# Optimization experiments

Hardware: AMD Instinct MI355X
Metric: run time of the kernel (lower is better)

The kernel has to match this reference:

```python
import jax, jax.numpy as jnp
import numpy as np

D = 768
B = 32
N = 768


def setup_inputs() -> dict:
    key = jax.random.key(0)
    k1, k2, k3, k4 = jax.random.split(key, 4)
    stdv = 1.0 / np.sqrt(D)
    X = jax.random.normal(k1, (B, N, D), dtype=jnp.float32)
    adj = jax.random.uniform(k2, (B, N, N), dtype=jnp.float32)
    W_l = jax.random.uniform(k3, (D, D), dtype=jnp.float32, minval=-stdv, maxval=stdv)
    W_l1 = jax.random.uniform(k4, (D, D), dtype=jnp.float32, minval=-stdv, maxval=stdv)
    return {"X": X, "adj": adj, "W_l": W_l, "W_l1": W_l1}


def _row_normalize(adj):
    # rowsum^-1 with inf -> 0 (rows summing to zero stay zero)
    rowsum = adj.sum(axis=-1, keepdims=True)  # [B, N, 1]
    r_inv = jnp.where(rowsum == 0, 0.0, 1.0 / rowsum)
    return adj * r_inv


def reference(X, adj, W_l, W_l1):
    # X: [B, N, D], adj: [B, N, N]
    adj_n = _row_normalize(adj)
    e1 = jnp.einsum('bnd,de->bne', X, W_l1)        # message transform
    e11 = jnp.einsum('bnm,bmd->bnd', adj_n, e1)    # aggregate
    X1 = jnp.einsum('bnd,de->bne', X, W_l)         # self transform
    h = X1 + e11
    return jax.nn.leaky_relu(h, negative_slope=0.01)
```

## Files before the change

kernel.cpp:

```cpp
#include <hip/hip_runtime.h>
#include <hip/hip_bf16.h>
#include <cstdint>
#include <cstddef>

#define BN_ROWS 24576
#define DD 768
#define BE (768*768)
#define BM 192
#define BN_T 192
#define BK 32
#define ABUF 12288
#define BUFSZ 24576

typedef __attribute__((ext_vector_type(8))) short bf16x8;
typedef __attribute__((ext_vector_type(4))) float f32x4;
typedef __attribute__((ext_vector_type(8))) unsigned short u16x8;

static __device__ __forceinline__ unsigned short f2bf(float f) {
  unsigned int u = __builtin_bit_cast(unsigned int, f);
  unsigned int lsb = (u >> 16) & 1u;
  u += 0x7fffu + lsb;
  return (unsigned short)(u >> 16);
}



#define PREP_CX 4096
#define PREP_WT 144
#define PREP_FL 288
#define PREP_AN 6144

__global__ __launch_bounds__(256) void prep(const float* __restrict__ X,
                                            const float* __restrict__ adj,
                                            const float* __restrict__ Wl,
                                            const float* __restrict__ Wl1,
                                            unsigned short* __restrict__ Xb,
                                            unsigned short* __restrict__ adjnb,
                                            unsigned short* __restrict__ WlT,
                                            unsigned short* __restrict__ Wl1T) {
  __shared__ float tile[64][65];
  const int bid = blockIdx.x;

  if (bid < PREP_CX) {
    const int n4 = (BN_ROWS * DD) / 4;
    for (int i = bid * 256 + threadIdx.x; i < n4; i += PREP_CX * 256) {
      float4 v = reinterpret_cast<const float4*>(X)[i];
      ushort4 o;
      o.x = f2bf(v.x); o.y = f2bf(v.y); o.z = f2bf(v.z); o.w = f2bf(v.w);
      reinterpret_cast<ushort4*>(Xb)[i] = o;
    }
  } else if (bid < PREP_CX + PREP_WT) {
    const int tb = bid - PREP_CX;
    const int tr = tb / 12, tc = tb % 12;
    const int c = threadIdx.x & 63, r0 = threadIdx.x >> 6;
    #pragma unroll
    for (int i = 0; i < 16; ++i) {
      int r = r0 + i * 4;
      tile[r][c] = Wl1[(size_t)(tr * 64 + r) * DD + tc * 64 + c];
    }
    __syncthreads();
    #pragma unroll
    for (int i = 0; i < 16; ++i) {
      int r2 = r0 + i * 4;
      Wl1T[(size_t)(tc * 64 + r2) * DD + tr * 64 + c] = f2bf(tile[c][r2]);
    }
  } else if (bid < PREP_CX + PREP_WT + PREP_FL) {
    const int b2 = bid - (PREP_CX + PREP_WT);
    const int wg = b2 * 4 + (threadIdx.x >> 6);
    const int lane = threadIdx.x & 63;
    const int d0 = (wg % 96) * 8;
    const int e = (wg / 96) * 64 + lane;
    u16x8 o;
    #pragma unroll
    for (int j = 0; j < 8; ++j)
      o[j] = f2bf(Wl[(size_t)(d0 + j) * DD + e]);
    const int base = ((e >> 4) * 24 + (d0 >> 5)) * 512
                   + ((e & 15) + (((d0 >> 3) & 3) << 4)) * 8;
    *reinterpret_cast<u16x8*>(WlT + base) = o;
  } else {
    const int rb = bid - (PREP_CX + PREP_WT + PREP_FL);
    const int wid = threadIdx.x >> 6, lane = threadIdx.x & 63;
    const int row = rb * 4 + wid;
    const float4* a = reinterpret_cast<const float4*>(adj + (size_t)row * DD);
    float4 v[3];
    float s = 0.f;
    #pragma unroll
    for (int i = 0; i < 3; ++i) {
      v[i] = a[i * 64 + lane];
      s += (v[i].x + v[i].y) + (v[i].z + v[i].w);
    }
    #pragma unroll
    for (int off = 32; off; off >>= 1) s += __shfl_down(s, off);
    s = __shfl(s, 0);
    float rinv = (s == 0.f) ? 0.f : 1.f / s;
    ushort4* o = reinterpret_cast<ushort4*>(adjnb + (size_t)row * DD);
    #pragma unroll
    for (int i = 0; i < 3; ++i) {
      ushort4 u;
      u.x = f2bf(v[i].x * rinv); u.y = f2bf(v[i].y * rinv);
      u.z = f2bf(v[i].z * rinv); u.w = f2bf(v[i].w * rinv);
      o[i * 64 + lane] = u;
    }
  }
}

__global__ __launch_bounds__(256, 2) void gemm_e1(
    const unsigned short* __restrict__ Xb,
    const unsigned short* __restrict__ W1T,
    unsigned short* __restrict__ e1T)
{
  __shared__ char smem[2 * BUFSZ];
  constexpr int NT = 24;
  const int tid = threadIdx.x, lane = tid & 63;
  const int wid = tid >> 6;
  const int wr = wid >> 1, wc = wid & 1;

  const int logical = (blockIdx.x & 7) * 64 + (blockIdx.x >> 3);
  const int mt = logical >> 2, nt = logical & 3;
  const int b = mt >> 2;
  const unsigned short* Ab0 = Xb + (size_t)mt * BM * DD;
  const unsigned short* Bb0 = W1T + (size_t)nt * BN_T * DD;

  const int r_in = lane >> 2;
  const int s_in = lane & 3;

  auto stage = [&](int s) {
    const int buf = (s & 1) * BUFSZ;
    #pragma unroll
    for (int i = 0; i < 6; ++i) {
      int chunk = wid * 6 + i;
      bool isA = chunk < 12;
      int c = isA ? chunk : chunk - 12;
      int row = c * 16 + r_in;
      int slot = s_in ^ ((row >> 1) & 3);
      const unsigned short* src = (isA ? Ab0 : Bb0) + (size_t)row * DD + s * BK + slot * 8;
      __builtin_amdgcn_global_load_lds(
          (const __attribute__((address_space(1))) void*)src,
          (__attribute__((address_space(3))) void*)(smem + buf + (isA ? 0 : ABUF) + c * 1024),
          16, 0, 0);
    }
  };

  const int ks = lane >> 4;
  auto frag = [&](int off, int row) -> bf16x8 {
    int slot = ks ^ ((row >> 1) & 3);
    return *reinterpret_cast<const bf16x8*>(smem + off + row * 64 + slot * 16);
  };

  f32x4 acc[6][6] = {};
  const int arow = wr * 96 + (lane & 15);
  const int brow = wc * 96 + (lane & 15);

  stage(0);
  for (int t = 0; t < NT; ++t) {
    asm volatile("s_waitcnt vmcnt(0)" ::: "memory");
    __builtin_amdgcn_s_barrier();
    if (t + 1 < NT) stage(t + 1);
    const int bufA = (t & 1) * BUFSZ;
    const int bufB = bufA + ABUF;
    bf16x8 a[6], bg[6];
    #pragma unroll
    for (int i = 0; i < 6; ++i) a[i] = frag(bufA, arow + i * 16);
    #pragma unroll
    for (int i = 0; i < 6; ++i) bg[i] = frag(bufB, brow + i * 16);
    __builtin_amdgcn_s_setprio(1);
    #pragma unroll
    for (int ni = 0; ni < 6; ++ni)
      #pragma unroll
      for (int mi = 0; mi < 6; ++mi)
        acc[mi][ni] = __builtin_amdgcn_mfma_f32_16x16x32_bf16(a[mi], bg[ni], acc[mi][ni], 0, 0, 0);
    __builtin_amdgcn_s_setprio(0);
  }

  unsigned short* ob = e1T + (size_t)b * BE;
  const int m0 = (mt & 3) * BM + wr * 96 + (lane >> 4) * 4;
  const int l15 = lane & 15;
  #pragma unroll
  for (int mi = 0; mi < 6; ++mi)
    #pragma unroll
    for (int ni = 0; ni < 6; ++ni) {
      int m = m0 + mi * 16;
      int cb = nt * 12 + wc * 6 + ni;
      int fa = (cb * 24 + (m >> 5)) * 512
             + (l15 + (((m >> 3) & 3) << 4)) * 8 + (m & 7);
      f32x4 v = acc[mi][ni];
      ushort4 o;
      o.x = f2bf(v[0]); o.y = f2bf(v[1]); o.z = f2bf(v[2]); o.w = f2bf(v[3]);
      *reinterpret_cast<ushort4*>(ob + fa) = o;
    }
}

__global__ __launch_bounds__(256, 2) void gemm_bg(
    const unsigned short* __restrict__ adjnb,
    const unsigned short* __restrict__ e1T,
    const unsigned short* __restrict__ Xb,
    const unsigned short* __restrict__ WlT,
    float* __restrict__ out)
{
  __shared__ char smem[24576];
  constexpr int NT = 48;
  const int tid = threadIdx.x, lane = tid & 63;
  const int wid = tid >> 6;
  const int wr = wid >> 1, wc = wid & 1;

  const int logical = (blockIdx.x & 7) * 64 + (blockIdx.x >> 3);
  const int b = logical >> 4;
  const int r = logical & 15;
  const int mt = r >> 2, nt = r & 3;
  const size_t bo = (size_t)b * BE;
  const unsigned short* A0 = adjnb + bo + (size_t)mt * BM * DD;
  const unsigned short* A1 = Xb + bo + (size_t)mt * BM * DD;
  const unsigned short* B0 = e1T + bo;
  const unsigned short* B1 = WlT;

  const int r_in = lane >> 2;
  const int s_in = lane & 3;
  const int colblk0 = nt * 12 + wc * 6;

  auto stage = [&](int s) {
    int sc = s < NT ? s : 0;
    const unsigned short* base = (sc >= 24) ? A1 : A0;
    int kk = (sc >= 24) ? sc - 24 : sc;
    const int buf = (s & 1) * 12288;
    #pragma unroll
    for (int i = 0; i < 3; ++i) {
      int chunk = wid * 3 + i;
      int row = chunk * 16 + r_in;
      int slot = s_in ^ ((row >> 1) & 3);
      const unsigned short* src = base + (size_t)row * DD + kk * BK + slot * 8;
      __builtin_amdgcn_global_load_lds(
          (const __attribute__((address_space(1))) void*)src,
          (__attribute__((address_space(3))) void*)(smem + buf + chunk * 1024),
          16, 0, 0);
    }
  };

  auto loadB = [&](int s, bf16x8* dst) {
    int sc = s < NT ? s : 0;
    const unsigned short* base = (sc >= 24) ? B1 : B0;
    int kk = (sc >= 24) ? sc - 24 : sc;
    #pragma unroll
    for (int ni = 0; ni < 6; ++ni)
      dst[ni] = *reinterpret_cast<const bf16x8*>(
          base + ((colblk0 + ni) * 24 + kk) * 512 + lane * 8);
  };

  const int ks = lane >> 4;
  auto rdA = [&](int off, int row) -> bf16x8 {
    int slot = ks ^ ((row >> 1) & 3);
    return *reinterpret_cast<const bf16x8*>(smem + off + row * 64 + slot * 16);
  };

  f32x4 acc[6][6] = {};
  const int arow = wr * 96 + (lane & 15);
  bf16x8 bA[6], bB[6];

  auto body = [&](int bufo, bf16x8* bfr) {
    #pragma unroll
    for (int mh = 0; mh < 2; ++mh) {
      bf16x8 a[3];
      #pragma unroll
      for (int i = 0; i < 3; ++i) a[i] = rdA(bufo, arow + mh * 48 + i * 16);
      __builtin_amdgcn_s_setprio(1);
      #pragma unroll
      for (int mi = 0; mi < 3; ++mi)
        #pragma unroll
        for (int ni = 0; ni < 6; ++ni)
          acc[mh * 3 + mi][ni] = __builtin_amdgcn_mfma_f32_16x16x32_bf16(
              a[mi], bfr[ni], acc[mh * 3 + mi][ni], 0, 0, 0);
      __builtin_amdgcn_s_setprio(0);
    }
  };

  stage(0); loadB(0, bA);
  for (int t = 0; t < NT; t += 2) {
    asm volatile("s_waitcnt vmcnt(6)" ::: "memory");
    __builtin_amdgcn_s_barrier();
    stage(t + 1); loadB(t + 1, bB);
    body(0, bA);
    asm volatile("s_waitcnt vmcnt(6)" ::: "memory");
    __builtin_amdgcn_s_barrier();
    stage(t + 2); loadB(t + 2, bA);
    body(12288, bB);
  }
  asm volatile("s_waitcnt vmcnt(0)" ::: "memory");

  float* ob = out + bo;
  const int m0 = mt * BM + wr * 96 + (lane >> 4) * 4;
  const int l15 = lane & 15;
  #pragma unroll
  for (int mi = 0; mi < 6; ++mi)
    #pragma unroll
    for (int ni = 0; ni < 6; ++ni) {
      int m = m0 + mi * 16;
      int n = nt * BN_T + wc * 96 + ni * 16 + l15;
      f32x4 v = acc[mi][ni];
      #pragma unroll
      for (int j = 0; j < 4; ++j) {
        float x = v[j];
        ob[(size_t)(m + j) * DD + n] = x > 0.f ? x : 0.01f * x;
      }
    }
}


extern "C" void kernel_launch(void* const* d_in, const int* in_sizes, int n_in,
                              void* d_out, int out_size, void* d_ws, size_t ws_size,
                              hipStream_t stream) {
  const float* X   = (const float*)d_in[0];
  const float* adj = (const float*)d_in[1];
  const float* Wl  = (const float*)d_in[2];
  const float* Wl1 = (const float*)d_in[3];
  float* out = (float*)d_out;

  char* ws = (char*)d_ws;
  const size_t SZ = (size_t)BN_ROWS * DD * 2;
  unsigned short* Xb    = (unsigned short*)(ws);
  unsigned short* adjnb = (unsigned short*)(ws + SZ);
  unsigned short* e1T   = (unsigned short*)(ws + 2 * SZ);
  unsigned short* WlT   = (unsigned short*)(ws + 3 * SZ);
  unsigned short* Wl1T  = (unsigned short*)(ws + 3 * SZ + (size_t)BE * 2);

  prep<<<PREP_CX + PREP_WT + PREP_FL + PREP_AN, 256, 0, stream>>>(
      X, adj, Wl, Wl1, Xb, adjnb, WlT, Wl1T);
  gemm_e1<<<512, 256, 0, stream>>>(Xb, Wl1T, e1T);
  gemm_bg<<<512, 256, 0, stream>>>(adjnb, e1T, Xb, WlT, out);
}
```

Measured before the change: 139.0 us.

## Fuse fp32-to-bf16 conversion and row normalization into GEMM A-tile loads

Drops the prep-stage bf16 copies of X and normalized adj. The GEMM kernels now load fp32 A tiles into registers, scale adj rows by a precomputed reciprocal row sum, convert to bf16 and write them to LDS, using a register-staged software pipeline. Prep keeps only the weight transposes and the per-row reciprocal sums. This removes writing and rereading two large bf16 intermediates, but doubles the bytes the GEMMs read from global memory for A, and adds VALU conversion work plus explicit waitcnt and barrier sequencing inside the main loops.

```diff
diff --git a/kernel.cpp b/kernel.cpp
--- a/kernel.cpp
+++ b/kernel.cpp
@@ -23,35 +23,35 @@
   return (unsigned short)(u >> 16);
 }
 
-
-
-#define PREP_CX 4096
+static __device__ __forceinline__ unsigned short f2bfv(float f) {
+  __hip_bfloat16 h = __float2bfloat16(f);
+  return __builtin_bit_cast(unsigned short, h);
+}
+
+static __device__ __forceinline__ bf16x8 cvt8(float4 u, float4 w, float sc) {
+  bf16x8 o;
+  o[0] = (short)f2bfv(u.x * sc); o[1] = (short)f2bfv(u.y * sc);
+  o[2] = (short)f2bfv(u.z * sc); o[3] = (short)f2bfv(u.w * sc);
+  o[4] = (short)f2bfv(w.x * sc); o[5] = (short)f2bfv(w.y * sc);
+  o[6] = (short)f2bfv(w.z * sc); o[7] = (short)f2bfv(w.w * sc);
+  return o;
+}
+
+
 #define PREP_WT 144
 #define PREP_FL 288
-#define PREP_AN 6144
-
-__global__ __launch_bounds__(256) void prep(const float* __restrict__ X,
-                                            const float* __restrict__ adj,
+#define PREP_RS 6144
+
+__global__ __launch_bounds__(256) void prep(const float* __restrict__ adj,
                                             const float* __restrict__ Wl,
                                             const float* __restrict__ Wl1,
-                                            unsigned short* __restrict__ Xb,
-                                            unsigned short* __restrict__ adjnb,
+                                            float* __restrict__ rinv,
                                             unsigned short* __restrict__ WlT,
                                             unsigned short* __restrict__ Wl1T) {
   __shared__ float tile[64][65];
   const int bid = blockIdx.x;
-
-  if (bid < PREP_CX) {
-    const int n4 = (BN_ROWS * DD) / 4;
-    for (int i = bid * 256 + threadIdx.x; i < n4; i += PREP_CX * 256) {
-      float4 v = reinterpret_cast<const float4*>(X)[i];
-      ushort4 o;
-      o.x = f2bf(v.x); o.y = f2bf(v.y); o.z = f2bf(v.z); o.w = f2bf(v.w);
-      reinterpret_cast<ushort4*>(Xb)[i] = o;
-    }
-  } else if (bid < PREP_CX + PREP_WT) {
-    const int tb = bid - PREP_CX;
-    const int tr = tb / 12, tc = tb % 12;
+  if (bid < PREP_WT) {
+    const int tr = bid / 12, tc = bid % 12;
     const int c = threadIdx.x & 63, r0 = threadIdx.x >> 6;
     #pragma unroll
     for (int i = 0; i < 16; ++i) {
@@ -64,8 +64,8 @@
       int r2 = r0 + i * 4;
       Wl1T[(size_t)(tc * 64 + r2) * DD + tr * 64 + c] = f2bf(tile[c][r2]);
     }
-  } else if (bid < PREP_CX + PREP_WT + PREP_FL) {
-    const int b2 = bid - (PREP_CX + PREP_WT);
+  } else if (bid < PREP_WT + PREP_FL) {
+    const int b2 = bid - PREP_WT;
     const int wg = b2 * 4 + (threadIdx.x >> 6);
     const int lane = threadIdx.x & 63;
     const int d0 = (wg % 96) * 8;
@@ -78,7 +78,7 @@
                    + ((e & 15) + (((d0 >> 3) & 3) << 4)) * 8;
     *reinterpret_cast<u16x8*>(WlT + base) = o;
   } else {
-    const int rb = bid - (PREP_CX + PREP_WT + PREP_FL);
+    const int rb = bid - (PREP_WT + PREP_FL);
     const int wid = threadIdx.x >> 6, lane = threadIdx.x & 63;
     const int row = rb * 4 + wid;
     const float4* a = reinterpret_cast<const float4*>(adj + (size_t)row * DD);
@@ -91,21 +91,12 @@
     }
     #pragma unroll
     for (int off = 32; off; off >>= 1) s += __shfl_down(s, off);
-    s = __shfl(s, 0);
-    float rinv = (s == 0.f) ? 0.f : 1.f / s;
-    ushort4* o = reinterpret_cast<ushort4*>(adjnb + (size_t)row * DD);
-    #pragma unroll
-    for (int i = 0; i < 3; ++i) {
-      ushort4 u;
-      u.x = f2bf(v[i].x * rinv); u.y = f2bf(v[i].y * rinv);
-      u.z = f2bf(v[i].z * rinv); u.w = f2bf(v[i].w * rinv);
-      o[i * 64 + lane] = u;
-    }
+    if (lane == 0) rinv[row] = (s == 0.f) ? 0.f : 1.f / s;
   }
 }
 
 __global__ __launch_bounds__(256, 2) void gemm_e1(
-    const unsigned short* __restrict__ Xb,
+    const float* __restrict__ X,
     const unsigned short* __restrict__ W1T,
     unsigned short* __restrict__ e1T)
 {
@@ -118,25 +109,44 @@
   const int logical = (blockIdx.x & 7) * 64 + (blockIdx.x >> 3);
   const int mt = logical >> 2, nt = logical & 3;
   const int b = mt >> 2;
-  const unsigned short* Ab0 = Xb + (size_t)mt * BM * DD;
-  const unsigned short* Bb0 = W1T + (size_t)nt * BN_T * DD;
+  const float* Ag = X + (size_t)mt * BM * DD;
+  const unsigned short* Bg = W1T + (size_t)nt * BN_T * DD;
 
   const int r_in = lane >> 2;
   const int s_in = lane & 3;
 
-  auto stage = [&](int s) {
+  float4 aR[3][2];
+  auto issueA = [&](int s) {
+    int kk = s < NT ? s : 0;
+    #pragma unroll
+    for (int i = 0; i < 3; ++i) {
+      int row = (wid * 3 + i) * 16 + r_in;
+      int slot = s_in ^ ((row >> 1) & 3);
+      const float4* p = reinterpret_cast<const float4*>(
+          Ag + (size_t)row * DD + kk * BK + slot * 8);
+      aR[i][0] = p[0];
+      aR[i][1] = p[1];
+    }
+  };
+  auto writeA = [&](int s) {
     const int buf = (s & 1) * BUFSZ;
     #pragma unroll
-    for (int i = 0; i < 6; ++i) {
-      int chunk = wid * 6 + i;
-      bool isA = chunk < 12;
-      int c = isA ? chunk : chunk - 12;
+    for (int i = 0; i < 3; ++i)
+      *reinterpret_cast<bf16x8*>(smem + buf + (wid * 3 + i) * 1024 + lane * 16) =
+          cvt8(aR[i][0], aR[i][1], 1.0f);
+  };
+  auto issueB = [&](int s) {
+    int kk = s < NT ? s : 0;
+    const int buf = (s & 1) * BUFSZ + ABUF;
+    #pragma unroll
+    for (int i = 0; i < 3; ++i) {
+      int c = wid * 3 + i;
       int row = c * 16 + r_in;
       int slot = s_in ^ ((row >> 1) & 3);
-      const unsigned short* src = (isA ? Ab0 : Bb0) + (size_t)row * DD + s * BK + slot * 8;
+      const unsigned short* src = Bg + (size_t)row * DD + kk * BK + slot * 8;
       __builtin_amdgcn_global_load_lds(
           (const __attribute__((address_space(1))) void*)src,
-          (__attribute__((address_space(3))) void*)(smem + buf + (isA ? 0 : ABUF) + c * 1024),
+          (__attribute__((address_space(3))) void*)(smem + buf + c * 1024),
           16, 0, 0);
     }
   };
@@ -151,11 +161,19 @@
   const int arow = wr * 96 + (lane & 15);
   const int brow = wc * 96 + (lane & 15);
 
-  stage(0);
+  issueA(0);
+  asm volatile("s_waitcnt vmcnt(0)" ::: "memory");
+  writeA(0);
+  issueB(0);
+  issueA(1);
+  asm volatile("s_waitcnt lgkmcnt(0)" ::: "memory");
+  __builtin_amdgcn_s_barrier();
+
   for (int t = 0; t < NT; ++t) {
-    asm volatile("s_waitcnt vmcnt(0)" ::: "memory");
+    asm volatile("s_waitcnt vmcnt(6)" ::: "memory");
     __builtin_amdgcn_s_barrier();
-    if (t + 1 < NT) stage(t + 1);
+    issueB(t + 1);
+
     const int bufA = (t & 1) * BUFSZ;
     const int bufB = bufA + ABUF;
     bf16x8 a[6], bg[6];
@@ -163,6 +181,7 @@
     for (int i = 0; i < 6; ++i) a[i] = frag(bufA, arow + i * 16);
     #pragma unroll
     for (int i = 0; i < 6; ++i) bg[i] = frag(bufB, brow + i * 16);
+
     __builtin_amdgcn_s_setprio(1);
     #pragma unroll
     for (int ni = 0; ni < 6; ++ni)
@@ -170,6 +189,11 @@
       for (int mi = 0; mi < 6; ++mi)
         acc[mi][ni] = __builtin_amdgcn_mfma_f32_16x16x32_bf16(a[mi], bg[ni], acc[mi][ni], 0, 0, 0);
     __builtin_amdgcn_s_setprio(0);
+
+    asm volatile("s_waitcnt vmcnt(3)" ::: "memory");
+    writeA(t + 1);
+    issueA(t + 2);
+    asm volatile("s_waitcnt lgkmcnt(0)" ::: "memory");
   }
 
   unsigned short* ob = e1T + (size_t)b * BE;
@@ -191,13 +215,14 @@
 }
 
 __global__ __launch_bounds__(256, 2) void gemm_bg(
-    const unsigned short* __restrict__ adjnb,
+    const float* __restrict__ adj,
+    const float* __restrict__ X,
+    const float* __restrict__ rinv,
     const unsigned short* __restrict__ e1T,
-    const unsigned short* __restrict__ Xb,
     const unsigned short* __restrict__ WlT,
     float* __restrict__ out)
 {
-  __shared__ char smem[24576];
+  __shared__ char smem[2 * 12288];
   constexpr int NT = 48;
   const int tid = threadIdx.x, lane = tid & 63;
   const int wid = tid >> 6;
@@ -208,8 +233,8 @@
   const int r = logical & 15;
   const int mt = r >> 2, nt = r & 3;
   const size_t bo = (size_t)b * BE;
-  const unsigned short* A0 = adjnb + bo + (size_t)mt * BM * DD;
-  const unsigned short* A1 = Xb + bo + (size_t)mt * BM * DD;
+  const float* A0 = adj + bo + (size_t)mt * BM * DD;
+  const float* A1 = X + (size_t)(b * 768 + mt * BM) * DD;
   const unsigned short* B0 = e1T + bo;
   const unsigned short* B1 = WlT;
 
@@ -217,24 +242,37 @@
   const int s_in = lane & 3;
   const int colblk0 = nt * 12 + wc * 6;
 
-  auto stage = [&](int s) {
+  float rinv3[3];
+  #pragma unroll
+  for (int i = 0; i < 3; ++i)
+    rinv3[i] = rinv[b * 768 + mt * BM + (wid * 3 + i) * 16 + r_in];
+
+  float4 aR[3][2];
+  auto issueA = [&](int s) {
     int sc = s < NT ? s : 0;
-    const unsigned short* base = (sc >= 24) ? A1 : A0;
+    const float* base = (sc >= 24) ? A1 : A0;
     int kk = (sc >= 24) ? sc - 24 : sc;
+    #pragma unroll
+    for (int i = 0; i < 3; ++i) {
+      int row = (wid * 3 + i) * 16 + r_in;
+      int slot = s_in ^ ((row >> 1) & 3);
+      const float4* p = reinterpret_cast<const float4*>(
+          base + (size_t)row * DD + kk * BK + slot * 8);
+      aR[i][0] = p[0];
+      aR[i][1] = p[1];
+    }
+  };
+  auto writeA = [&](int s) {
+    int sc = s < NT ? s : 0;
+    const bool isAdj = sc < 24;
     const int buf = (s & 1) * 12288;
     #pragma unroll
     for (int i = 0; i < 3; ++i) {
-      int chunk = wid * 3 + i;
-      int row = chunk * 16 + r_in;
-      int slot = s_in ^ ((row >> 1) & 3);
-      const unsigned short* src = base + (size_t)row * DD + kk * BK + slot * 8;
-      __builtin_amdgcn_global_load_lds(
-          (const __attribute__((address_space(1))) void*)src,
-          (__attribute__((address_space(3))) void*)(smem + buf + chunk * 1024),
-          16, 0, 0);
-    }
-  };
-
+      float scl = isAdj ? rinv3[i] : 1.0f;
+      *reinterpret_cast<bf16x8*>(smem + buf + (wid * 3 + i) * 1024 + lane * 16) =
+          cvt8(aR[i][0], aR[i][1], scl);
+    }
+  };
   auto loadB = [&](int s, bf16x8* dst) {
     int sc = s < NT ? s : 0;
     const unsigned short* base = (sc >= 24) ? B1 : B0;
@@ -272,18 +310,31 @@
     }
   };
 
-  stage(0); loadB(0, bA);
+  issueA(0);
+  asm volatile("s_waitcnt vmcnt(0)" ::: "memory");
+  writeA(0);
+  loadB(0, bA);
+  issueA(1);
+  asm volatile("s_waitcnt lgkmcnt(0)" ::: "memory");
+  __builtin_amdgcn_s_barrier();
+
   for (int t = 0; t < NT; t += 2) {
-    asm volatile("s_waitcnt vmcnt(6)" ::: "memory");
-    __builtin_amdgcn_s_barrier();
-    stage(t + 1); loadB(t + 1, bB);
+    loadB(t + 1, bB);
     body(0, bA);
     asm volatile("s_waitcnt vmcnt(6)" ::: "memory");
+    writeA(t + 1);
+    issueA(t + 2);
+    asm volatile("s_waitcnt lgkmcnt(0)" ::: "memory");
     __builtin_amdgcn_s_barrier();
-    stage(t + 2); loadB(t + 2, bA);
+
+    loadB(t + 2, bA);
     body(12288, bB);
+    asm volatile("s_waitcnt vmcnt(6)" ::: "memory");
+    writeA(t + 2);
+    issueA(t + 3);
+    asm volatile("s_waitcnt lgkmcnt(0)" ::: "memory");
+    __builtin_amdgcn_s_barrier();
   }
-  asm volatile("s_waitcnt vmcnt(0)" ::: "memory");
 
   float* ob = out + bo;
   const int m0 = mt * BM + wr * 96 + (lane >> 4) * 4;
@@ -315,14 +366,12 @@
 
   char* ws = (char*)d_ws;
   const size_t SZ = (size_t)BN_ROWS * DD * 2;
-  unsigned short* Xb    = (unsigned short*)(ws);
-  unsigned short* adjnb = (unsigned short*)(ws + SZ);
-  unsigned short* e1T   = (unsigned short*)(ws + 2 * SZ);
-  unsigned short* WlT   = (unsigned short*)(ws + 3 * SZ);
-  unsigned short* Wl1T  = (unsigned short*)(ws + 3 * SZ + (size_t)BE * 2);
-
-  prep<<<PREP_CX + PREP_WT + PREP_FL + PREP_AN, 256, 0, stream>>>(
-      X, adj, Wl, Wl1, Xb, adjnb, WlT, Wl1T);
-  gemm_e1<<<512, 256, 0, stream>>>(Xb, Wl1T, e1T);
-  gemm_bg<<<512, 256, 0, stream>>>(adjnb, e1T, Xb, WlT, out);
-}
+  unsigned short* e1T  = (unsigned short*)(ws);
+  unsigned short* WlT  = (unsigned short*)(ws + SZ);
+  unsigned short* Wl1T = (unsigned short*)(ws + SZ + (size_t)BE * 2);
+  float* rinv          = (float*)(ws + SZ + 2 * (size_t)BE * 2);
+
+  prep<<<PREP_WT + PREP_FL + PREP_RS, 256, 0, stream>>>(adj, Wl, Wl1, rinv, WlT, Wl1T);
+  gemm_e1<<<512, 256, 0, stream>>>(X, Wl1T, e1T);
+  gemm_bg<<<512, 256, 0, stream>>>(adj, X, rinv, e1T, WlT, out);
+}
```

Measured after the change: 134.4 us, median of 3. 1.03x faster.
